# Optimization experiments

Measured on AMD Instinct MI355X. Metric: run time of the kernel, lower is better.

The kernel has to match this reference:

```python
import jax, jax.numpy as jnp
import numpy as np

OUT, GROUPS, GRID = 4096, 1, 8   # 2^bits = 8 -> 3-bit codes
IN = 4096
B, S = 4, 2048

def setup_inputs() -> dict:
    key = jax.random.key(0)
    k1, k2, k3 = jax.random.split(key, 3)
    x = jax.random.normal(k1, (B, S, IN), dtype=jnp.float32)
    quant_grid = jax.random.normal(k2, (OUT, GROUPS, GRID), dtype=jnp.float32) * 0.02
    weight_codes = jax.random.randint(k3, (OUT, GROUPS, IN // GROUPS), 0, GRID, dtype=jnp.int32)
    return {"x": x, "quant_grid": quant_grid, "weight_codes": weight_codes}

def reference(x, quant_grid, weight_codes):
    # Dequantize: per-(row, group) codebook lookup -> full weight [OUT, IN]
    W = jnp.take_along_axis(quant_grid, weight_codes, axis=-1)  # [OUT, GROUPS, IN//GROUPS]
    W = W.reshape(W.shape[0], -1)                               # [OUT, IN]
    # y = X @ W.T
    return jnp.einsum('bsi,oi->bso', x, W)
```

## Files before the change

### kernel.cpp

```cpp
#include <hip/hip_runtime.h>


#define M_DIM 8192
#define N_DIM 4096
#define K_DIM 4096
#define BK 128
#define NKT (K_DIM / BK)

typedef __attribute__((ext_vector_type(4))) int int32x4;

#define AS1 __attribute__((address_space(1)))
#define AS3 __attribute__((address_space(3)))

__device__ __forceinline__ void gl_lds16(const void* g, void* l) {
    __builtin_amdgcn_global_load_lds((const AS1 void*)g, (AS3 void*)l, 16, 0, 0);
}

__global__ __launch_bounds__(256) void quant_x(const float* __restrict__ X,
                                               char* __restrict__ XQ,
                                               float* __restrict__ SX) {
    const int row = blockIdx.x;
    const int t = threadIdx.x;
    const float4* xp = (const float4*)(X + (size_t)row * K_DIM);
    float4 v[4];
    float mx = 0.0f;
#pragma unroll
    for (int i = 0; i < 4; ++i) {
        v[i] = xp[t * 4 + i];
        mx = fmaxf(mx, fmaxf(fmaxf(fabsf(v[i].x), fabsf(v[i].y)),
                             fmaxf(fabsf(v[i].z), fabsf(v[i].w))));
    }
#pragma unroll
    for (int off = 1; off < 64; off <<= 1)
        mx = fmaxf(mx, __shfl_xor(mx, off));
    __shared__ float wmx[4];
    if ((t & 63) == 0) wmx[t >> 6] = mx;
    __syncthreads();
    mx = fmaxf(fmaxf(wmx[0], wmx[1]), fmaxf(wmx[2], wmx[3]));
    const float inv = 127.0f / mx;
    int4 o4;
    int* po = (int*)&o4;
#pragma unroll
    for (int i = 0; i < 4; ++i) {
        int q0 = (int)rintf(v[i].x * inv);
        int q1 = (int)rintf(v[i].y * inv);
        int q2 = (int)rintf(v[i].z * inv);
        int q3 = (int)rintf(v[i].w * inv);
        po[i] = (q0 & 255) | ((q1 & 255) << 8) | ((q2 & 255) << 16) | ((q3 & 255) << 24);
    }
    ((int4*)(XQ + (size_t)row * K_DIM))[t] = o4;
    if (t == 0) SX[row] = mx * (1.0f / 127.0f);
}

__global__ __launch_bounds__(256) void quant_w(const int* __restrict__ CD,
                                               const float* __restrict__ G,
                                               char* __restrict__ WQ,
                                               float* __restrict__ SW) {
    const int o = blockIdx.x;
    __shared__ int gq[8];
    if (threadIdx.x == 0) {
        float g[8], mx = 0.0f;
#pragma unroll
        for (int j = 0; j < 8; ++j) { g[j] = G[o * 8 + j]; mx = fmaxf(mx, fabsf(g[j])); }
        mx = fmaxf(mx, 1e-20f);
        const float inv = 127.0f / mx;
        SW[o] = mx * (1.0f / 127.0f);
#pragma unroll
        for (int j = 0; j < 8; ++j) gq[j] = ((int)rintf(g[j] * inv)) & 255;
    }
    __syncthreads();
    const int4* cp = (const int4*)(CD + (size_t)o * K_DIM);
    int* wp = (int*)(WQ + (size_t)o * K_DIM);
#pragma unroll
    for (int r = 0; r < 4; ++r) {
        int idx = r * 256 + threadIdx.x;
        int4 c = cp[idx];
        wp[idx] = gq[c.x] | (gq[c.y] << 8) | (gq[c.z] << 16) | (gq[c.w] << 24);
    }
}

__global__ __launch_bounds__(512, 2) void gemm8(const char* __restrict__ A,
                                                const char* __restrict__ B,
                                                const float* __restrict__ SX,
                                                const float* __restrict__ SW,
                                                float* __restrict__ C) {
    __shared__ char As[2][2][128 * 128];
    __shared__ char Bs[2][2][128 * 128];

    const int tid = threadIdx.x;
    const int lane = tid & 63;
    const int wid = tid >> 6;
    const int wm = wid >> 2;
    const int wn = wid & 3;
    const int bh = wn >> 1;

    int wg = blockIdx.x;
    wg = (wg & 7) * (gridDim.x >> 3) + (wg >> 3);
    const int ntn = N_DIM / 256;
    const int bm = (wg / ntn) * 256;
    const int bn = (wg % ntn) * 256;

    const int fr = lane & 15;
    const int swzb = (fr & 7) << 4;
    const int offk0 = fr * 128 + (((lane >> 4) << 4) ^ swzb);
    const int offk1 = offk0 ^ 64;
    const int bwoffB = (wn & 1) * 8192;

    const int row0 = tid >> 3;
    const int sl = (((tid & 7) ^ (row0 & 7)) << 4);

#define STG(GP, RB, KT, LD) do {                                                   \
        const int kb_ = (((KT) < NKT) ? (KT) : 0) * BK;                            \
        gl_lds16((GP) + (size_t)((RB) + row0) * K_DIM + kb_ + sl,                  \
                 (LD) + wid * 1024);                                               \
        gl_lds16((GP) + (size_t)((RB) + row0 + 64) * K_DIM + kb_ + sl,             \
                 (LD) + 8192 + wid * 1024);                                        \
    } while (0)

#define RD_A(B_, MH_)                                                              \
    _Pragma("unroll") for (int m = 0; m < 4; ++m) {                                \
        fa[(MH_) * 4 + m][0] = *(const int32x4*)&As[B_][wm][(MH_) * 8192 + m * 2048 + offk0]; \
        fa[(MH_) * 4 + m][1] = *(const int32x4*)&As[B_][wm][(MH_) * 8192 + m * 2048 + offk1]; \
    }

#define RD_B(B_, NH_)                                                              \
    _Pragma("unroll") for (int n = 0; n < 2; ++n) {                                \
        fb[(NH_) * 2 + n][0] = *(const int32x4*)&Bs[B_][bh][bwoffB + (NH_) * 4096 + n * 2048 + offk0]; \
        fb[(NH_) * 2 + n][1] = *(const int32x4*)&Bs[B_][bh][bwoffB + (NH_) * 4096 + n * 2048 + offk1]; \
    }

#define MF(MH_, NH_)                                                               \
    _Pragma("unroll") for (int ks = 0; ks < 2; ++ks)                               \
    _Pragma("unroll") for (int m = 0; m < 4; ++m)                                  \
    _Pragma("unroll") for (int n = 0; n < 2; ++n)                                  \
        acc[(MH_) * 4 + m][(NH_) * 2 + n] = __builtin_amdgcn_mfma_i32_16x16x64_i8( \
            fa[(MH_) * 4 + m][ks], fb[(NH_) * 2 + n][ks],                          \
            acc[(MH_) * 4 + m][(NH_) * 2 + n], 0, 0, 0);

#define PH_MID                                                                     \
    __builtin_amdgcn_s_setprio(1);

#define PH_END                                                                     \
    __builtin_amdgcn_s_setprio(0);                                                 \
    __builtin_amdgcn_sched_barrier(0);                                             \
    __builtin_amdgcn_s_barrier();

#define PH_ENDW                                                                    \
    __builtin_amdgcn_s_setprio(0);                                                 \
    __builtin_amdgcn_sched_barrier(0);                                             \
    asm volatile("s_waitcnt vmcnt(6)" ::: "memory");                               \
    __builtin_amdgcn_s_barrier();

    int32x4 acc[8][4] = {};
    int32x4 fa[8][2];
    int32x4 fb[4][2];

    STG(A, bm,       0, &As[0][0][0]);
    STG(A, bm + 128, 0, &As[0][1][0]);
    STG(B, bn,       0, &Bs[0][0][0]);
    STG(B, bn + 128, 0, &Bs[0][1][0]);
    STG(B, bn,       1, &Bs[1][0][0]);
    STG(B, bn + 128, 1, &Bs[1][1][0]);
    STG(A, bm,       1, &As[1][0][0]);
    asm volatile("s_waitcnt vmcnt(6)" ::: "memory");
    __builtin_amdgcn_s_barrier();

    for (int j = 0; j < NKT / 2; ++j) {
        const int o = 2 * j + 1, e2 = 2 * j + 2, o2 = 2 * j + 3;
        RD_A(0, 0) RD_B(0, 0)
        STG(A, bm + 128, o, &As[1][1][0]);
        PH_MID MF(0, 0) PH_END
        RD_B(0, 1)
        STG(B, bn, e2, &Bs[0][0][0]);
        PH_MID MF(0, 1) PH_END
        RD_A(0, 1)
        STG(B, bn + 128, e2, &Bs[0][1][0]);
        PH_MID MF(1, 0) PH_END
        STG(A, bm, e2, &As[0][0][0]);
        PH_MID MF(1, 1) PH_ENDW
        RD_A(1, 0) RD_B(1, 0)
        STG(A, bm + 128, e2, &As[0][1][0]);
        PH_MID MF(0, 0) PH_END
        RD_B(1, 1)
        STG(B, bn, o2, &Bs[1][0][0]);
        PH_MID MF(0, 1) PH_END
        RD_A(1, 1)
        STG(B, bn + 128, o2, &Bs[1][1][0]);
        PH_MID MF(1, 0) PH_END
        STG(A, bm, o2, &As[1][0][0]);
        PH_MID MF(1, 1) PH_ENDW
    }
    asm volatile("s_waitcnt vmcnt(0)" ::: "memory");

    const int crow0 = bm + wm * 128 + ((lane >> 4) << 2);
    const int ccol0 = bn + wn * 64 + (lane & 15);
    float swc[4];
#pragma unroll
    for (int ni = 0; ni < 4; ++ni) swc[ni] = SW[ccol0 + ni * 16];
#pragma unroll
    for (int mi = 0; mi < 8; ++mi)
#pragma unroll
        for (int r = 0; r < 4; ++r) {
            const float sxr = SX[crow0 + mi * 16 + r];
#pragma unroll
            for (int ni = 0; ni < 4; ++ni)
                C[(size_t)(crow0 + mi * 16 + r) * N_DIM + ccol0 + ni * 16] =
                    (float)acc[mi][ni][r] * sxr * swc[ni];
        }
}

__global__ __launch_bounds__(256) void fb_gemm(const float* __restrict__ X,
                                               const float* __restrict__ G,
                                               const int* __restrict__ CD,
                                               float* __restrict__ Y) {
    __shared__ float xs[16][64];
    __shared__ float ws[16][64];
    const int bm = blockIdx.y << 6, bn = blockIdx.x << 6;
    const int tid = threadIdx.x;
    const int tn = tid & 15, tm = tid >> 4;
    float acc[4][4] = {};
    for (int k0 = 0; k0 < K_DIM; k0 += 16) {
#pragma unroll
        for (int r = 0; r < 4; ++r) {
            int e = r * 256 + tid;
            int mm = e >> 4, kk = e & 15;
            xs[kk][mm] = X[(size_t)(bm + mm) * K_DIM + k0 + kk];
            int code = CD[(size_t)(bn + mm) * K_DIM + k0 + kk];
            ws[kk][mm] = G[(bn + mm) * 8 + code];
        }
        __syncthreads();
#pragma unroll
        for (int kk = 0; kk < 16; ++kk)
#pragma unroll
            for (int i = 0; i < 4; ++i)
#pragma unroll
                for (int j = 0; j < 4; ++j)
                    acc[i][j] += xs[kk][tm * 4 + i] * ws[kk][tn * 4 + j];
        __syncthreads();
    }
#pragma unroll
    for (int i = 0; i < 4; ++i)
#pragma unroll
        for (int j = 0; j < 4; ++j)
            Y[(size_t)(bm + tm * 4 + i) * N_DIM + bn + tn * 4 + j] = acc[i][j];
}

extern "C" void kernel_launch(void* const* d_in, const int* in_sizes, int n_in,
                              void* d_out, int out_size, void* d_ws, size_t ws_size,
                              hipStream_t stream) {
    const float* x = (const float*)d_in[0];
    const float* qg = (const float*)d_in[1];
    const int* wc = (const int*)d_in[2];
    float* y = (float*)d_out;

    const size_t sx_off = 0;
    const size_t sw_off = (size_t)M_DIM * 4;
    const size_t xq_off = (size_t)(M_DIM + N_DIM) * 4;
    const size_t wq_off = xq_off + (size_t)M_DIM * K_DIM;
    const size_t need = wq_off + (size_t)N_DIM * K_DIM;

    if (ws_size >= need) {
        float* sx = (float*)((char*)d_ws + sx_off);
        float* sw = (float*)((char*)d_ws + sw_off);
        char* xq = (char*)d_ws + xq_off;
        char* wq = (char*)d_ws + wq_off;
        hipLaunchKernelGGL(quant_x, dim3(M_DIM), dim3(256), 0, stream, x, xq, sx);
        hipLaunchKernelGGL(quant_w, dim3(N_DIM), dim3(256), 0, stream, wc, qg, wq, sw);
        const int nwg = (M_DIM / 256) * (N_DIM / 256);
        hipLaunchKernelGGL(gemm8, dim3(nwg), dim3(512), 0, stream,
                           xq, wq, sx, sw, y);
    } else {
        hipLaunchKernelGGL(fb_gemm, dim3(N_DIM / 64, M_DIM / 64), dim3(256), 0, stream,
                           x, qg, wc, y);
    }
}
```

Baseline: 182.2 us.

## Shrink int8 GEMM tile to 128x256 with BK=64 for higher occupancy

The int8 MFMA GEMM tile goes from 256x256 with K-step 128 to 128x256 with K-step 64. LDS use drops from 128KB to 48KB per block, and the accumulator registers are halved so four blocks can be resident per CU instead of two. The LDS swizzle, the staging schedule and the waitcnt depths are reworked to match. In exchange, arithmetic intensity per block falls, so there is more global and LDS traffic per MFMA and more loop-iteration overhead.

```diff
diff --git a/kernel.cpp b/kernel.cpp
--- a/kernel.cpp
+++ b/kernel.cpp
@@ -4,7 +4,7 @@
 #define M_DIM 8192
 #define N_DIM 4096
 #define K_DIM 4096
-#define BK 128
+#define BK 64
 #define NKT (K_DIM / BK)
 
 typedef __attribute__((ext_vector_type(4))) int int32x4;
@@ -79,66 +79,57 @@
     }
 }
 
-__global__ __launch_bounds__(512, 2) void gemm8(const char* __restrict__ A,
+__global__ __launch_bounds__(512, 4) void gemm8(const char* __restrict__ A,
                                                 const char* __restrict__ B,
                                                 const float* __restrict__ SX,
                                                 const float* __restrict__ SW,
                                                 float* __restrict__ C) {
-    __shared__ char As[2][2][128 * 128];
-    __shared__ char Bs[2][2][128 * 128];
+    __shared__ char As[2][128 * 64];
+    __shared__ char Bs[2][256 * 64];
 
     const int tid = threadIdx.x;
     const int lane = tid & 63;
     const int wid = tid >> 6;
     const int wm = wid >> 2;
     const int wn = wid & 3;
-    const int bh = wn >> 1;
 
     int wg = blockIdx.x;
     wg = (wg & 7) * (gridDim.x >> 3) + (wg >> 3);
     const int ntn = N_DIM / 256;
-    const int bm = (wg / ntn) * 256;
+    const int bm = (wg / ntn) * 128;
     const int bn = (wg % ntn) * 256;
 
     const int fr = lane & 15;
-    const int swzb = (fr & 7) << 4;
-    const int offk0 = fr * 128 + (((lane >> 4) << 4) ^ swzb);
-    const int offk1 = offk0 ^ 64;
-    const int bwoffB = (wn & 1) * 8192;
-
-    const int row0 = tid >> 3;
-    const int sl = (((tid & 7) ^ (row0 & 7)) << 4);
-
-#define STG(GP, RB, KT, LD) do {                                                   \
-        const int kb_ = (((KT) < NKT) ? (KT) : 0) * BK;                            \
-        gl_lds16((GP) + (size_t)((RB) + row0) * K_DIM + kb_ + sl,                  \
-                 (LD) + wid * 1024);                                               \
-        gl_lds16((GP) + (size_t)((RB) + row0 + 64) * K_DIM + kb_ + sl,             \
-                 (LD) + 8192 + wid * 1024);                                        \
-    } while (0)
-
-#define RD_A(B_, MH_)                                                              \
-    _Pragma("unroll") for (int m = 0; m < 4; ++m) {                                \
-        fa[(MH_) * 4 + m][0] = *(const int32x4*)&As[B_][wm][(MH_) * 8192 + m * 2048 + offk0]; \
-        fa[(MH_) * 4 + m][1] = *(const int32x4*)&As[B_][wm][(MH_) * 8192 + m * 2048 + offk1]; \
-    }
-
-#define RD_B(B_, NH_)                                                              \
-    _Pragma("unroll") for (int n = 0; n < 2; ++n) {                                \
-        fb[(NH_) * 2 + n][0] = *(const int32x4*)&Bs[B_][bh][bwoffB + (NH_) * 4096 + n * 2048 + offk0]; \
-        fb[(NH_) * 2 + n][1] = *(const int32x4*)&Bs[B_][bh][bwoffB + (NH_) * 4096 + n * 2048 + offk1]; \
-    }
-
-#define MF(MH_, NH_)                                                               \
-    _Pragma("unroll") for (int ks = 0; ks < 2; ++ks)                               \
-    _Pragma("unroll") for (int m = 0; m < 4; ++m)                                  \
+    const int g = lane >> 4;
+    const int offk = fr * 64 + ((g ^ ((fr >> 1) & 3)) << 4);
+    const int awoff = wm * 4096;
+    const int bwoff = wn * 4096;
+
+    const int row0 = tid >> 2;
+    const int sl = (((tid & 3) ^ ((row0 >> 1) & 3)) << 4);
+    const char* gA  = A + (size_t)(bm + row0) * K_DIM + sl;
+    const char* gB0 = B + (size_t)(bn + row0) * K_DIM + sl;
+    const char* gB1 = B + (size_t)(bn + 128 + row0) * K_DIM + sl;
+
+#define KB(KT) ((((KT) < NKT) ? (KT) : 0) * BK)
+#define STGA(BUF, KT) gl_lds16(gA + KB(KT), &As[BUF][0] + wid * 1024);
+#define STGB(BUF, H, KT) gl_lds16(gB##H + KB(KT), &Bs[BUF][(H) * 8192] + wid * 1024);
+
+#define RD_A(BUF, MH)                                                              \
+    _Pragma("unroll") for (int m = 0; m < 2; ++m)                                  \
+        fa[(MH) * 2 + m] = *(const int32x4*)&As[BUF][awoff + ((MH) * 2 + m) * 1024 + offk];
+
+#define RD_B(BUF, NH)                                                              \
     _Pragma("unroll") for (int n = 0; n < 2; ++n)                                  \
-        acc[(MH_) * 4 + m][(NH_) * 2 + n] = __builtin_amdgcn_mfma_i32_16x16x64_i8( \
-            fa[(MH_) * 4 + m][ks], fb[(NH_) * 2 + n][ks],                          \
-            acc[(MH_) * 4 + m][(NH_) * 2 + n], 0, 0, 0);
-
-#define PH_MID                                                                     \
-    __builtin_amdgcn_s_setprio(1);
+        fb[(NH) * 2 + n] = *(const int32x4*)&Bs[BUF][bwoff + ((NH) * 2 + n) * 1024 + offk];
+
+#define MF(MH, NH)                                                                 \
+    _Pragma("unroll") for (int m = 0; m < 2; ++m)                                  \
+    _Pragma("unroll") for (int n = 0; n < 2; ++n)                                  \
+        acc[(MH) * 2 + m][(NH) * 2 + n] = __builtin_amdgcn_mfma_i32_16x16x64_i8(   \
+            fa[(MH) * 2 + m], fb[(NH) * 2 + n], acc[(MH) * 2 + m][(NH) * 2 + n], 0, 0, 0);
+
+#define PH_MID __builtin_amdgcn_s_setprio(1);
 
 #define PH_END                                                                     \
     __builtin_amdgcn_s_setprio(0);                                                 \
@@ -148,57 +139,53 @@
 #define PH_ENDW                                                                    \
     __builtin_amdgcn_s_setprio(0);                                                 \
     __builtin_amdgcn_sched_barrier(0);                                             \
-    asm volatile("s_waitcnt vmcnt(6)" ::: "memory");                               \
+    asm volatile("s_waitcnt vmcnt(2)" ::: "memory");                               \
     __builtin_amdgcn_s_barrier();
 
-    int32x4 acc[8][4] = {};
-    int32x4 fa[8][2];
-    int32x4 fb[4][2];
-
-    STG(A, bm,       0, &As[0][0][0]);
-    STG(A, bm + 128, 0, &As[0][1][0]);
-    STG(B, bn,       0, &Bs[0][0][0]);
-    STG(B, bn + 128, 0, &Bs[0][1][0]);
-    STG(B, bn,       1, &Bs[1][0][0]);
-    STG(B, bn + 128, 1, &Bs[1][1][0]);
-    STG(A, bm,       1, &As[1][0][0]);
-    asm volatile("s_waitcnt vmcnt(6)" ::: "memory");
+    int32x4 acc[4][4] = {};
+    int32x4 fa[4];
+    int32x4 fb[4];
+
+    STGB(0, 0, 0)
+    STGB(0, 1, 0)
+    STGA(0, 0)
+    STGB(1, 0, 1)
+    STGB(1, 1, 1)
+    asm volatile("s_waitcnt vmcnt(2)" ::: "memory");
     __builtin_amdgcn_s_barrier();
 
     for (int j = 0; j < NKT / 2; ++j) {
         const int o = 2 * j + 1, e2 = 2 * j + 2, o2 = 2 * j + 3;
         RD_A(0, 0) RD_B(0, 0)
-        STG(A, bm + 128, o, &As[1][1][0]);
+        STGA(1, o)
         PH_MID MF(0, 0) PH_END
         RD_B(0, 1)
-        STG(B, bn, e2, &Bs[0][0][0]);
         PH_MID MF(0, 1) PH_END
         RD_A(0, 1)
-        STG(B, bn + 128, e2, &Bs[0][1][0]);
+        STGB(0, 0, e2)
         PH_MID MF(1, 0) PH_END
-        STG(A, bm, e2, &As[0][0][0]);
+        STGB(0, 1, e2)
         PH_MID MF(1, 1) PH_ENDW
         RD_A(1, 0) RD_B(1, 0)
-        STG(A, bm + 128, e2, &As[0][1][0]);
+        STGA(0, e2)
         PH_MID MF(0, 0) PH_END
         RD_B(1, 1)
-        STG(B, bn, o2, &Bs[1][0][0]);
         PH_MID MF(0, 1) PH_END
         RD_A(1, 1)
-        STG(B, bn + 128, o2, &Bs[1][1][0]);
+        STGB(1, 0, o2)
         PH_MID MF(1, 0) PH_END
-        STG(A, bm, o2, &As[1][0][0]);
+        STGB(1, 1, o2)
         PH_MID MF(1, 1) PH_ENDW
     }
     asm volatile("s_waitcnt vmcnt(0)" ::: "memory");
 
-    const int crow0 = bm + wm * 128 + ((lane >> 4) << 2);
-    const int ccol0 = bn + wn * 64 + (lane & 15);
+    const int crow0 = bm + wm * 64 + (g << 2);
+    const int ccol0 = bn + wn * 64 + fr;
     float swc[4];
 #pragma unroll
     for (int ni = 0; ni < 4; ++ni) swc[ni] = SW[ccol0 + ni * 16];
 #pragma unroll
-    for (int mi = 0; mi < 8; ++mi)
+    for (int mi = 0; mi < 4; ++mi)
 #pragma unroll
         for (int r = 0; r < 4; ++r) {
             const float sxr = SX[crow0 + mi * 16 + r];
@@ -266,7 +253,7 @@
         char* wq = (char*)d_ws + wq_off;
         hipLaunchKernelGGL(quant_x, dim3(M_DIM), dim3(256), 0, stream, x, xq, sx);
         hipLaunchKernelGGL(quant_w, dim3(N_DIM), dim3(256), 0, stream, wc, qg, wq, sw);
-        const int nwg = (M_DIM / 256) * (N_DIM / 256);
+        const int nwg = (M_DIM / 128) * (N_DIM / 256);
         hipLaunchKernelGGL(gemm8, dim3(nwg), dim3(512), 0, stream,
                            xq, wq, sx, sw, y);
     } else {
```

Result: slower. 199.4 us (+9.5%).

## Double-buffer MFMA fragment registers and reorder int8 GEMM main-loop schedule

Applied to the files above, without the earlier changes.

Splits the A/B fragment registers into two ping-pong sets so LDS reads for the next quadrant are issued before or during the current quadrant's MFMAs. The order of quadrant visits and global-to-LDS staging is reshuffled, and the partial vmcnt(6) waits are replaced by full vmcnt(0) waits at mid-iteration points. The aim is to hide LDS read latency behind matrix math. The cost is higher register pressure, and the stricter waits may expose global load latency.

```diff
diff --git a/kernel.cpp b/kernel.cpp
--- a/kernel.cpp
+++ b/kernel.cpp
@@ -117,80 +117,78 @@
                  (LD) + 8192 + wid * 1024);                                        \
     } while (0)
 
-#define RD_A(B_, MH_)                                                              \
+#define RDA(FA, B_, MH_)                                                           \
     _Pragma("unroll") for (int m = 0; m < 4; ++m) {                                \
-        fa[(MH_) * 4 + m][0] = *(const int32x4*)&As[B_][wm][(MH_) * 8192 + m * 2048 + offk0]; \
-        fa[(MH_) * 4 + m][1] = *(const int32x4*)&As[B_][wm][(MH_) * 8192 + m * 2048 + offk1]; \
-    }
-
-#define RD_B(B_, NH_)                                                              \
+        FA[m * 2 + 0] = *(const int32x4*)&As[B_][wm][(MH_) * 8192 + m * 2048 + offk0]; \
+        FA[m * 2 + 1] = *(const int32x4*)&As[B_][wm][(MH_) * 8192 + m * 2048 + offk1]; \
+    }
+
+#define RDB(FB, B_, NH_)                                                           \
     _Pragma("unroll") for (int n = 0; n < 2; ++n) {                                \
-        fb[(NH_) * 2 + n][0] = *(const int32x4*)&Bs[B_][bh][bwoffB + (NH_) * 4096 + n * 2048 + offk0]; \
-        fb[(NH_) * 2 + n][1] = *(const int32x4*)&Bs[B_][bh][bwoffB + (NH_) * 4096 + n * 2048 + offk1]; \
-    }
-
-#define MF(MH_, NH_)                                                               \
+        FB[n * 2 + 0] = *(const int32x4*)&Bs[B_][bh][bwoffB + (NH_) * 4096 + n * 2048 + offk0]; \
+        FB[n * 2 + 1] = *(const int32x4*)&Bs[B_][bh][bwoffB + (NH_) * 4096 + n * 2048 + offk1]; \
+    }
+
+#define MFQ(FA, FB, MH_, NH_)                                                      \
+    __builtin_amdgcn_s_setprio(1);                                                 \
     _Pragma("unroll") for (int ks = 0; ks < 2; ++ks)                               \
     _Pragma("unroll") for (int m = 0; m < 4; ++m)                                  \
     _Pragma("unroll") for (int n = 0; n < 2; ++n)                                  \
         acc[(MH_) * 4 + m][(NH_) * 2 + n] = __builtin_amdgcn_mfma_i32_16x16x64_i8( \
-            fa[(MH_) * 4 + m][ks], fb[(NH_) * 2 + n][ks],                          \
-            acc[(MH_) * 4 + m][(NH_) * 2 + n], 0, 0, 0);
-
-#define PH_MID                                                                     \
-    __builtin_amdgcn_s_setprio(1);
-
-#define PH_END                                                                     \
-    __builtin_amdgcn_s_setprio(0);                                                 \
-    __builtin_amdgcn_sched_barrier(0);                                             \
-    __builtin_amdgcn_s_barrier();
-
-#define PH_ENDW                                                                    \
-    __builtin_amdgcn_s_setprio(0);                                                 \
-    __builtin_amdgcn_sched_barrier(0);                                             \
-    asm volatile("s_waitcnt vmcnt(6)" ::: "memory");                               \
-    __builtin_amdgcn_s_barrier();
+            FA[m * 2 + ks], FB[n * 2 + ks],                                        \
+            acc[(MH_) * 4 + m][(NH_) * 2 + n], 0, 0, 0);                           \
+    __builtin_amdgcn_s_setprio(0);
+
+#define FENCE __builtin_amdgcn_sched_barrier(0);
+#define BAR   __builtin_amdgcn_s_barrier();
+#define VM0   asm volatile("s_waitcnt vmcnt(0)" ::: "memory");
 
     int32x4 acc[8][4] = {};
-    int32x4 fa[8][2];
-    int32x4 fb[4][2];
-
+    int32x4 fa0[8], fa1[8];
+    int32x4 fb0[4], fb1[4];
+
+    STG(B, bn,       0, &Bs[0][0][0]);
+    STG(B, bn + 128, 0, &Bs[0][1][0]);
     STG(A, bm,       0, &As[0][0][0]);
     STG(A, bm + 128, 0, &As[0][1][0]);
-    STG(B, bn,       0, &Bs[0][0][0]);
-    STG(B, bn + 128, 0, &Bs[0][1][0]);
-    STG(B, bn,       1, &Bs[1][0][0]);
+    STG(A, bm,       1, &As[1][0][0]);
+    STG(A, bm + 128, 1, &As[1][1][0]);
     STG(B, bn + 128, 1, &Bs[1][1][0]);
-    STG(A, bm,       1, &As[1][0][0]);
     asm volatile("s_waitcnt vmcnt(6)" ::: "memory");
-    __builtin_amdgcn_s_barrier();
+    BAR
+    RDA(fa0, 0, 0)
+    RDB(fb0, 0, 0)
 
     for (int j = 0; j < NKT / 2; ++j) {
         const int o = 2 * j + 1, e2 = 2 * j + 2, o2 = 2 * j + 3;
-        RD_A(0, 0) RD_B(0, 0)
-        STG(A, bm + 128, o, &As[1][1][0]);
-        PH_MID MF(0, 0) PH_END
-        RD_B(0, 1)
+        STG(B, bn, o, &Bs[1][0][0]);
+        RDB(fb1, 0, 1)
+        MFQ(fa0, fb0, 0, 0) FENCE BAR
+        RDA(fa1, 0, 1)
+        MFQ(fa0, fb1, 0, 1) FENCE VM0 BAR
+        STG(A, bm, e2, &As[0][0][0]);
+        RDA(fa0, 1, 0)
+        MFQ(fa1, fb1, 1, 1) FENCE BAR
+        STG(B, bn + 128, e2, &Bs[0][1][0]);
+        MFQ(fa1, fb0, 1, 0)
+        RDB(fb0, 1, 0)
+        FENCE BAR
+        STG(A, bm + 128, e2, &As[0][1][0]);
         STG(B, bn, e2, &Bs[0][0][0]);
-        PH_MID MF(0, 1) PH_END
-        RD_A(0, 1)
-        STG(B, bn + 128, e2, &Bs[0][1][0]);
-        PH_MID MF(1, 0) PH_END
-        STG(A, bm, e2, &As[0][0][0]);
-        PH_MID MF(1, 1) PH_ENDW
-        RD_A(1, 0) RD_B(1, 0)
-        STG(A, bm + 128, e2, &As[0][1][0]);
-        PH_MID MF(0, 0) PH_END
-        RD_B(1, 1)
-        STG(B, bn, o2, &Bs[1][0][0]);
-        PH_MID MF(0, 1) PH_END
-        RD_A(1, 1)
+        RDB(fb1, 1, 1)
+        MFQ(fa0, fb0, 0, 0) FENCE BAR
+        RDA(fa1, 1, 1)
+        MFQ(fa0, fb1, 0, 1) FENCE VM0 BAR
+        STG(A, bm, o2, &As[1][0][0]);
+        RDA(fa0, 0, 0)
+        MFQ(fa1, fb1, 1, 1) FENCE BAR
+        STG(A, bm + 128, o2, &As[1][1][0]);
         STG(B, bn + 128, o2, &Bs[1][1][0]);
-        PH_MID MF(1, 0) PH_END
-        STG(A, bm, o2, &As[1][0][0]);
-        PH_MID MF(1, 1) PH_ENDW
-    }
-    asm volatile("s_waitcnt vmcnt(0)" ::: "memory");
+        MFQ(fa1, fb0, 1, 0)
+        RDB(fb0, 0, 0)
+        FENCE BAR
+    }
+    VM0
 
     const int crow0 = bm + wm * 128 + ((lane >> 4) << 2);
     const int ccol0 = bn + wn * 64 + (lane & 15);
```

Measured after the change: 256.2 us. 1.41x slower.
